# Performance work log

Hardware: AMD Instinct MI355X
Metric: run time of the kernel (lower is better)

Reference implementation:

```python
import jax, jax.numpy as jnp
import numpy as np

R = 16
ALPHA = 32
SCALING = ALPHA / R  # 2.0
E = 8
TOP_K = 2


def setup_inputs() -> dict:
    key = jax.random.key(0)
    ks = jax.random.split(key, 5)
    B, S, D = 4, 2048, 4096
    x = jax.random.normal(ks[0], (B, S, D), dtype=jnp.float32)
    base_W = jax.random.normal(ks[1], (D, D), dtype=jnp.float32) * 0.02
    router_W = jax.random.normal(ks[2], (E, D), dtype=jnp.float32) * 0.02
    lora_A = jax.random.normal(ks[3], (E, D, R), dtype=jnp.float32) * 0.02
    lora_B = jax.random.normal(ks[4], (E, R, D), dtype=jnp.float32) * 0.02
    return {"x": x, "base_W": base_W, "router_W": router_W,
            "lora_A": lora_A, "lora_B": lora_B}


def reference(x, base_W, router_W, lora_A, lora_B):
    # base linear: y = x @ W^T  (nn.Linear, bias=False)
    base = jnp.einsum('bsd,od->bso', x, base_W)

    # router logits and top-2 routing (softmax in fp32, as in torch)
    logits = jnp.einsum('bsd,ed->bse', x, router_W)
    probs = jax.nn.softmax(logits.astype(jnp.float32), axis=-1)  # [B,S,E]
    top_vals, top_idx = jax.lax.top_k(probs, TOP_K)               # [B,S,2]
    rw = top_vals / jnp.sum(top_vals, axis=-1, keepdims=True)
    # scatter top-2 weights into dense [B,S,E] combine matrix
    w_dense = jnp.sum(jax.nn.one_hot(top_idx, E, dtype=rw.dtype) * rw[..., None],
                      axis=-2).astype(x.dtype)                    # [B,S,E]

    # expert LoRA: out_n = sum_e w_ne * (x_n @ A_e @ B_e)
    # apply routing weight at rank-r stage (B_e linear => same math),
    # avoiding the [B,S,E,D] intermediate.
    mid = jnp.einsum('bsd,edr->bser', x, lora_A)                  # [B,S,E,r]
    mid = mid * w_dense[..., None]
    inc = jnp.einsum('bser,erd->bsd', mid, lora_B)                # [B,S,D]

    return base + inc * SCALING
```

## Files before the change

kernel.cpp:

```cpp
#include <hip/hip_runtime.h>
#include <math.h>

#define DI __device__ __forceinline__

typedef __attribute__((ext_vector_type(4))) float  f32x4;
typedef __attribute__((ext_vector_type(4))) short  s16x4;
typedef __attribute__((ext_vector_type(8))) short  s16x8;
typedef __attribute__((ext_vector_type(4))) float  ffrag;
typedef s16x8 bfrag;

constexpr int NT = 8192;
constexpr int D  = 4096;
constexpr int NE = 8;
constexpr int KE = 128;
constexpr int KX = D + KE;

DI short f2bf(float f) {
  unsigned u = __builtin_bit_cast(unsigned, f);
  u += 0x7FFFu + ((u >> 16) & 1u);
  return (short)(u >> 16);
}
DI float bf2f(short h) {
  unsigned u = ((unsigned)(unsigned short)h) << 16;
  return __builtin_bit_cast(float, u);
}

#define GLOAD16(gp, lp)                                                        \
  __builtin_amdgcn_global_load_lds(                                            \
      (const __attribute__((address_space(1))) void*)(gp),                     \
      (__attribute__((address_space(3))) void*)(lp), 16, 0, 0)

__global__ void moe_k_detect(const unsigned* __restrict__ x, int* __restrict__ flag) {
  int l = threadIdx.x;
  int cnt = 0;
  for (int i = l; i < 2048; i += 64) {
    unsigned e = (x[i] >> 23) & 0xFFu;
    cnt += (e >= 110u && e <= 140u) ? 1 : 0;
  }
#pragma unroll
  for (int o = 32; o; o >>= 1) cnt += __shfl_xor(cnt, o);
  if (l == 0) flag[0] = (cnt > 1024) ? 0 : 1;
}

__global__ __launch_bounds__(256)
void moe_k_prep(const void* __restrict__ wp, const void* __restrict__ lAp,
                const void* __restrict__ lBp, const int* __restrict__ flag,
                short* __restrict__ Wb, short* __restrict__ Abt) {
  const bool bf = flag[0] != 0;
  int b = blockIdx.x, t = threadIdx.x;
  if (b < 8192) {
    int tid = b * 256 + t;
    int row = tid >> 9;
    int col = (tid & 511) << 3;
    s16x8 o;
    if (!bf) {
      const float* Wf = (const float*)wp;
      f32x4 v0 = *(const f32x4*)&Wf[(size_t)row * 4096 + col];
      f32x4 v1 = *(const f32x4*)&Wf[(size_t)row * 4096 + col + 4];
      o[0] = f2bf(v0[0]); o[1] = f2bf(v0[1]); o[2] = f2bf(v0[2]); o[3] = f2bf(v0[3]);
      o[4] = f2bf(v1[0]); o[5] = f2bf(v1[1]); o[6] = f2bf(v1[2]); o[7] = f2bf(v1[3]);
    } else {
      o = *(const s16x8*)&((const short*)wp)[(size_t)row * 4096 + col];
    }
    *(s16x8*)&Wb[(size_t)row * KX + col] = o;
  } else if (b < 8208) {
    int d = (b - 8192) * 256 + t;
    for (int j0 = 0; j0 < KE; j0 += 8) {
      s16x8 o;
#pragma unroll
      for (int i = 0; i < 8; ++i) {
        float v = bf ? bf2f(((const short*)lBp)[(size_t)(j0 + i) * 4096 + d])
                     : ((const float*)lBp)[(size_t)(j0 + i) * 4096 + d];
        o[i] = f2bf(2.0f * v);
      }
      *(s16x8*)&Wb[(size_t)d * KX + 4096 + j0] = o;
    }
  } else {
    int j = b - 8208;
    int e = j >> 4, r = j & 15;
    for (int d = t; d < 4096; d += 256) {
      size_t src = ((size_t)e * 4096 + d) * 16 + r;
      short v = bf ? ((const short*)lAp)[src] : f2bf(((const float*)lAp)[src]);
      Abt[(size_t)j * 4096 + d] = v;
    }
  }
}

__global__ __launch_bounds__(256)
void moe_k_xrouter(const void* __restrict__ xp, const void* __restrict__ rp,
                   const int* __restrict__ flag, short* __restrict__ Xb,
                   float* __restrict__ wdense) {
  const bool bf = flag[0] != 0;
  int t = threadIdx.x, wv = t >> 6, l = t & 63;
  int n = blockIdx.x * 4 + wv;
  float acc[NE];
#pragma unroll
  for (int e = 0; e < NE; ++e) acc[e] = 0.f;
  const float* xf = (const float*)xp;
  const short* xh = (const short*)xp;
  const float* rf = (const float*)rp;
  const short* rh = (const short*)rp;
  for (int it = 0; it < 16; ++it) {
    int d = it * 256 + l * 4;
    float x0, x1, x2, x3;
    s16x4 xo;
    if (!bf) {
      f32x4 v = *(const f32x4*)&xf[(size_t)n * D + d];
      x0 = v[0]; x1 = v[1]; x2 = v[2]; x3 = v[3];
      xo[0] = f2bf(x0); xo[1] = f2bf(x1); xo[2] = f2bf(x2); xo[3] = f2bf(x3);
    } else {
      xo = *(const s16x4*)&xh[(size_t)n * D + d];
      x0 = bf2f(xo[0]); x1 = bf2f(xo[1]); x2 = bf2f(xo[2]); x3 = bf2f(xo[3]);
    }
    *(s16x4*)&Xb[(size_t)n * KX + d] = xo;
#pragma unroll
    for (int e = 0; e < NE; ++e) {
      if (!bf) {
        f32x4 w = *(const f32x4*)&rf[(size_t)e * D + d];
        acc[e] += x0 * w[0] + x1 * w[1] + x2 * w[2] + x3 * w[3];
      } else {
        s16x4 w = *(const s16x4*)&rh[(size_t)e * D + d];
        acc[e] += x0 * bf2f(w[0]) + x1 * bf2f(w[1]) + x2 * bf2f(w[2]) + x3 * bf2f(w[3]);
      }
    }
  }
#pragma unroll
  for (int e = 0; e < NE; ++e) {
#pragma unroll
    for (int o = 32; o; o >>= 1) acc[e] += __shfl_xor(acc[e], o);
  }
  float m = acc[0];
#pragma unroll
  for (int e = 1; e < NE; ++e) m = fmaxf(m, acc[e]);
  float p[NE];
#pragma unroll
  for (int e = 0; e < NE; ++e) p[e] = __expf(acc[e] - m);
  int i1 = 0; float v1 = p[0];
#pragma unroll
  for (int e = 1; e < NE; ++e) { if (p[e] > v1) { v1 = p[e]; i1 = e; } }
  int i2 = 0; float v2 = -1.f;
#pragma unroll
  for (int e = 0; e < NE; ++e) { if (e != i1 && p[e] > v2) { v2 = p[e]; i2 = e; } }
  float inv = 1.f / (v1 + v2);
  if (l < NE) {
    float w = (l == i1) ? v1 * inv : ((l == i2) ? v2 * inv : 0.f);
    wdense[(size_t)n * NE + l] = w;
  }
}

__global__ __launch_bounds__(256)
void moe_k_mid2(const short* __restrict__ Xb, const short* __restrict__ Abt,
                const float* __restrict__ wdense, short* __restrict__ XbW) {
  __shared__ __align__(16) short LDS[16384];
  const int t = threadIdx.x, l = t & 63, wv = t >> 6;
  const int wr = wv >> 1, wc = wv & 1;
  const int lr = l & 15, kq = l >> 4;
  const int m0 = (blockIdx.x >> 1) * 64;
  const int j0 = (blockIdx.x & 1) * 64;

  ffrag acc[2][2];
#pragma unroll
  for (int i = 0; i < 2; ++i)
#pragma unroll
    for (int j = 0; j < 2; ++j)
#pragma unroll
      for (int q = 0; q < 4; ++q) acc[i][j][q] = 0.f;

  const int srow = t >> 2, sslot = t & 3;
#define MSTAGE(kt_)                                                            \
  do {                                                                         \
    int _k0 = (kt_) * 32, _b = ((kt_) & 3) * 4096;                             \
    GLOAD16(&Xb[(size_t)(m0 + srow) * KX + _k0 + sslot * 8], &LDS[_b + t * 8]);\
    GLOAD16(&Abt[(size_t)(j0 + srow) * 4096 + _k0 + sslot * 8],                \
            &LDS[_b + 2048 + t * 8]);                                          \
  } while (0)

  MSTAGE(0); MSTAGE(1); MSTAGE(2);
  constexpr int NKT = 128;

  for (int kt = 0; kt < NKT; ++kt) {
    if (kt + 2 < NKT)      asm volatile("s_waitcnt vmcnt(4)" ::: "memory");
    else if (kt + 1 < NKT) asm volatile("s_waitcnt vmcnt(2)" ::: "memory");
    else                   asm volatile("s_waitcnt vmcnt(0)" ::: "memory");
    __builtin_amdgcn_s_barrier();
    __builtin_amdgcn_sched_barrier(0);

    const int bufs = (kt & 3) * 4096;
    const short* As = &LDS[bufs + (wr * 32 + lr) * 32 + kq * 8];
    const short* Bs = &LDS[bufs + 2048 + (wc * 32 + lr) * 32 + kq * 8];
    bfrag a0 = *(const bfrag*)&As[0];
    bfrag a1 = *(const bfrag*)&As[512];
    bfrag b0 = *(const bfrag*)&Bs[0];
    bfrag b1 = *(const bfrag*)&Bs[512];
    if (kt + 3 < NKT) MSTAGE(kt + 3);
    asm volatile("" ::: "memory");
    acc[0][0] = __builtin_amdgcn_mfma_f32_16x16x32_bf16(b0, a0, acc[0][0], 0, 0, 0);
    acc[0][1] = __builtin_amdgcn_mfma_f32_16x16x32_bf16(b1, a0, acc[0][1], 0, 0, 0);
    acc[1][0] = __builtin_amdgcn_mfma_f32_16x16x32_bf16(b0, a1, acc[1][0], 0, 0, 0);
    acc[1][1] = __builtin_amdgcn_mfma_f32_16x16x32_bf16(b1, a1, acc[1][1], 0, 0, 0);
  }

#pragma unroll
  for (int m = 0; m < 2; ++m)
#pragma unroll
    for (int n = 0; n < 2; ++n) {
      int gr = m0 + wr * 32 + m * 16 + lr;
      int jb = j0 + wc * 32 + n * 16 + kq * 4;
      int e  = jb >> 4;
      float w = wdense[(size_t)gr * NE + e];
      s16x4 o;
#pragma unroll
      for (int q = 0; q < 4; ++q) o[q] = f2bf(acc[m][n][q] * w);
      *(s16x4*)&XbW[(size_t)gr * KX + 4096 + jb] = o;
    }
#undef MSTAGE
}

__global__ __launch_bounds__(512, 2)
void moe_k_main8(const short* __restrict__ Xb, const short* __restrict__ Wb,
                 const int* __restrict__ flag, void* __restrict__ outp) {
  __shared__ __align__(16) short LDS[65536];
  const int t = threadIdx.x;
  const int l = t & 63;
  const int wv = t >> 6;
  const int wr = wv >> 2;
  const int wc = wv & 3;
  const int lr = l & 15;
  const int kq = l >> 4;

  int wg = blockIdx.x;
  int swz = (wg & 7) * 64 + (wg >> 3);
  const int tm = (swz >> 4) * 256;
  const int tn = (swz & 15) * 256;

  ffrag acc[8][4];
#pragma unroll
  for (int i = 0; i < 8; ++i)
#pragma unroll
    for (int j = 0; j < 4; ++j)
#pragma unroll
      for (int q = 0; q < 4; ++q) acc[i][j][q] = 0.f;

#define STAGE_A(kt_)                                                           \
  do {                                                                         \
    int _k0 = (kt_) * 32, _b = ((kt_) & 3) * 16384;                            \
    _Pragma("unroll")                                                          \
    for (int _i = 0; _i < 2; ++_i) {                                           \
      int _c = _i * 512 + t;                                                   \
      int _r = _c >> 2;                                                        \
      int _kc = (_c & 3) ^ ((_r >> 1) & 3);                                    \
      GLOAD16(&Xb[(size_t)(tm + _r) * KX + _k0 + _kc * 8], &LDS[_b + _c * 8]); \
    }                                                                          \
  } while (0)
#define STAGE_B(kt_)                                                           \
  do {                                                                         \
    int _k0 = (kt_) * 32, _b = ((kt_) & 3) * 16384 + 8192;                     \
    _Pragma("unroll")                                                          \
    for (int _i = 0; _i < 2; ++_i) {                                           \
      int _c = _i * 512 + t;                                                   \
      int _r = _c >> 2;                                                        \
      int _kc = (_c & 3) ^ ((_r >> 1) & 3);                                    \
      GLOAD16(&Wb[(size_t)(tn + _r) * KX + _k0 + _kc * 8], &LDS[_b + _c * 8]); \
    }                                                                          \
  } while (0)

  STAGE_A(0); STAGE_B(0);
  STAGE_A(1); STAGE_B(1);
  STAGE_A(2); STAGE_B(2);

  constexpr int NKT = KX / 32;

  const int kx = kq ^ ((lr >> 1) & 3);
  const int aofs = (wr * 128 + lr) * 32 + kx * 8;
  const int bofs = 8192 + (wc * 64 + lr) * 32 + kx * 8;

#define MFMA_ROW(mi, av)                                                           \
  acc[mi][0] = __builtin_amdgcn_mfma_f32_16x16x32_bf16(b0, av, acc[mi][0], 0, 0, 0); \
  acc[mi][1] = __builtin_amdgcn_mfma_f32_16x16x32_bf16(b1, av, acc[mi][1], 0, 0, 0); \
  acc[mi][2] = __builtin_amdgcn_mfma_f32_16x16x32_bf16(b2, av, acc[mi][2], 0, 0, 0); \
  acc[mi][3] = __builtin_amdgcn_mfma_f32_16x16x32_bf16(b3, av, acc[mi][3], 0, 0, 0);

  for (int kt = 0; kt < NKT; ++kt) {
    if (kt + 2 < NKT)      asm volatile("s_waitcnt vmcnt(8)" ::: "memory");
    else if (kt + 1 < NKT) asm volatile("s_waitcnt vmcnt(4)" ::: "memory");
    else                   asm volatile("s_waitcnt vmcnt(0)" ::: "memory");
    __builtin_amdgcn_s_barrier();
    __builtin_amdgcn_sched_barrier(0);

    const int bufs = (kt & 3) * 16384;
    const short* Ab = &LDS[bufs + aofs];
    const short* Bb = &LDS[bufs + bofs];

    bfrag b0 = *(const bfrag*)&Bb[0];
    bfrag b1 = *(const bfrag*)&Bb[512];
    bfrag b2 = *(const bfrag*)&Bb[1024];
    bfrag b3 = *(const bfrag*)&Bb[1536];
    bfrag a0 = *(const bfrag*)&Ab[0];
    bfrag a1 = *(const bfrag*)&Ab[512];
    bfrag a2 = *(const bfrag*)&Ab[1024];
    bfrag a3 = *(const bfrag*)&Ab[1536];
    if (kt + 3 < NKT) STAGE_A(kt + 3);
    asm volatile("" ::: "memory");
    __builtin_amdgcn_s_barrier();
    __builtin_amdgcn_sched_barrier(0);
    __builtin_amdgcn_s_setprio(1);
    MFMA_ROW(0, a0) MFMA_ROW(1, a1) MFMA_ROW(2, a2) MFMA_ROW(3, a3)
    __builtin_amdgcn_s_setprio(0);

    bfrag a4 = *(const bfrag*)&Ab[2048];
    bfrag a5 = *(const bfrag*)&Ab[2560];
    bfrag a6 = *(const bfrag*)&Ab[3072];
    bfrag a7 = *(const bfrag*)&Ab[3584];
    if (kt + 3 < NKT) STAGE_B(kt + 3);
    asm volatile("" ::: "memory");
    __builtin_amdgcn_s_barrier();
    __builtin_amdgcn_sched_barrier(0);
    __builtin_amdgcn_s_setprio(1);
    MFMA_ROW(4, a4) MFMA_ROW(5, a5) MFMA_ROW(6, a6) MFMA_ROW(7, a7)
    __builtin_amdgcn_s_setprio(0);
  }

  const bool bf = flag[0] != 0;
  float* of = (float*)outp;
  unsigned short* oh = (unsigned short*)outp;
#pragma unroll
  for (int m = 0; m < 8; ++m)
#pragma unroll
    for (int n = 0; n < 4; ++n) {
      int gr = tm + wr * 128 + m * 16 + lr;
      int gc = tn + wc * 64 + n * 16 + kq * 4;
      if (!bf) {
        *(f32x4*)&of[(size_t)gr * D + gc] = acc[m][n];
      } else {
        s16x4 o;
#pragma unroll
        for (int q = 0; q < 4; ++q) o[q] = f2bf(acc[m][n][q]);
        *(s16x4*)&oh[(size_t)gr * D + gc] = o;
      }
    }
#undef STAGE_A
#undef STAGE_B
#undef MFMA_ROW
}

extern "C" void kernel_launch(void* const* d_in, const int* in_sizes, int n_in,
                              void* d_out, int out_size, void* d_ws, size_t ws_size,
                              hipStream_t stream) {
  const void* x  = d_in[0];
  const void* bw = d_in[1];
  const void* rw = d_in[2];
  const void* lA = d_in[3];
  const void* lB = d_in[4];

  char* ws = (char*)d_ws;
  const size_t XB_BYTES  = (size_t)NT * KX * 2;
  const size_t WB_BYTES  = (size_t)D * KX * 2;
  const size_t ABT_BYTES = (size_t)KE * D * 2;
  const size_t WD_BYTES  = (size_t)NT * NE * 4;
  const size_t NEED = 256 + XB_BYTES + WB_BYTES + ABT_BYTES + WD_BYTES;
  if (ws_size < NEED) return;

  int*   flag   = (int*)ws;
  short* Xb     = (short*)(ws + 256);
  short* Wb     = (short*)(ws + 256 + XB_BYTES);
  short* Abt    = (short*)(ws + 256 + XB_BYTES + WB_BYTES);
  float* wdense = (float*)(ws + 256 + XB_BYTES + WB_BYTES + ABT_BYTES);

  hipLaunchKernelGGL(moe_k_detect, dim3(1), dim3(64), 0, stream,
                     (const unsigned*)x, flag);
  hipLaunchKernelGGL(moe_k_prep, dim3(8336), dim3(256), 0, stream,
                     bw, lA, lB, flag, Wb, Abt);
  hipLaunchKernelGGL(moe_k_xrouter, dim3(NT / 4), dim3(256), 0, stream,
                     x, rw, flag, Xb, wdense);
  hipLaunchKernelGGL(moe_k_mid2, dim3(256), dim3(256), 0, stream,
                     Xb, Abt, wdense, Xb);
  hipLaunchKernelGGL(moe_k_main8, dim3(512), dim3(512), 0, stream,
                     Xb, Wb, flag, d_out);
}
```

Baseline: 403.7 us.

## Shrink main GEMM tile to 128x128 with double buffering and merge prep kernels

Result: slower. 521.0 us (+29.1%).

```diff
diff --git a/kernel.cpp b/kernel.cpp
--- a/kernel.cpp
+++ b/kernel.cpp
@@ -43,9 +43,11 @@
 }
 
 __global__ __launch_bounds__(256)
-void moe_k_prep(const void* __restrict__ wp, const void* __restrict__ lAp,
-                const void* __restrict__ lBp, const int* __restrict__ flag,
-                short* __restrict__ Wb, short* __restrict__ Abt) {
+void moe_k_prep_xr(const void* __restrict__ wp, const void* __restrict__ lAp,
+                   const void* __restrict__ lBp, const void* __restrict__ xp,
+                   const void* __restrict__ rp, const int* __restrict__ flag,
+                   short* __restrict__ Wb, short* __restrict__ Abt,
+                   short* __restrict__ Xb, float* __restrict__ wdense) {
   const bool bf = flag[0] != 0;
   int b = blockIdx.x, t = threadIdx.x;
   if (b < 8192) {
@@ -75,7 +77,7 @@
       }
       *(s16x8*)&Wb[(size_t)d * KX + 4096 + j0] = o;
     }
-  } else {
+  } else if (b < 8336) {
     int j = b - 8208;
     int e = j >> 4, r = j & 15;
     for (int d = t; d < 4096; d += 256) {
@@ -83,68 +85,62 @@
       short v = bf ? ((const short*)lAp)[src] : f2bf(((const float*)lAp)[src]);
       Abt[(size_t)j * 4096 + d] = v;
     }
-  }
-}
-
-__global__ __launch_bounds__(256)
-void moe_k_xrouter(const void* __restrict__ xp, const void* __restrict__ rp,
-                   const int* __restrict__ flag, short* __restrict__ Xb,
-                   float* __restrict__ wdense) {
-  const bool bf = flag[0] != 0;
-  int t = threadIdx.x, wv = t >> 6, l = t & 63;
-  int n = blockIdx.x * 4 + wv;
-  float acc[NE];
-#pragma unroll
-  for (int e = 0; e < NE; ++e) acc[e] = 0.f;
-  const float* xf = (const float*)xp;
-  const short* xh = (const short*)xp;
-  const float* rf = (const float*)rp;
-  const short* rh = (const short*)rp;
-  for (int it = 0; it < 16; ++it) {
-    int d = it * 256 + l * 4;
-    float x0, x1, x2, x3;
-    s16x4 xo;
-    if (!bf) {
-      f32x4 v = *(const f32x4*)&xf[(size_t)n * D + d];
-      x0 = v[0]; x1 = v[1]; x2 = v[2]; x3 = v[3];
-      xo[0] = f2bf(x0); xo[1] = f2bf(x1); xo[2] = f2bf(x2); xo[3] = f2bf(x3);
-    } else {
-      xo = *(const s16x4*)&xh[(size_t)n * D + d];
-      x0 = bf2f(xo[0]); x1 = bf2f(xo[1]); x2 = bf2f(xo[2]); x3 = bf2f(xo[3]);
-    }
-    *(s16x4*)&Xb[(size_t)n * KX + d] = xo;
+  } else {
+    int wv = t >> 6, l = t & 63;
+    int n = (b - 8336) * 4 + wv;
+    float acc[NE];
+#pragma unroll
+    for (int e = 0; e < NE; ++e) acc[e] = 0.f;
+    const float* xf = (const float*)xp;
+    const short* xh = (const short*)xp;
+    const float* rf = (const float*)rp;
+    const short* rh = (const short*)rp;
+    for (int it = 0; it < 16; ++it) {
+      int d = it * 256 + l * 4;
+      float x0, x1, x2, x3;
+      s16x4 xo;
+      if (!bf) {
+        f32x4 v = *(const f32x4*)&xf[(size_t)n * D + d];
+        x0 = v[0]; x1 = v[1]; x2 = v[2]; x3 = v[3];
+        xo[0] = f2bf(x0); xo[1] = f2bf(x1); xo[2] = f2bf(x2); xo[3] = f2bf(x3);
+      } else {
+        xo = *(const s16x4*)&xh[(size_t)n * D + d];
+        x0 = bf2f(xo[0]); x1 = bf2f(xo[1]); x2 = bf2f(xo[2]); x3 = bf2f(xo[3]);
+      }
+      *(s16x4*)&Xb[(size_t)n * KX + d] = xo;
+#pragma unroll
+      for (int e = 0; e < NE; ++e) {
+        if (!bf) {
+          f32x4 w = *(const f32x4*)&rf[(size_t)e * D + d];
+          acc[e] += x0 * w[0] + x1 * w[1] + x2 * w[2] + x3 * w[3];
+        } else {
+          s16x4 w = *(const s16x4*)&rh[(size_t)e * D + d];
+          acc[e] += x0 * bf2f(w[0]) + x1 * bf2f(w[1]) + x2 * bf2f(w[2]) + x3 * bf2f(w[3]);
+        }
+      }
+    }
 #pragma unroll
     for (int e = 0; e < NE; ++e) {
-      if (!bf) {
-        f32x4 w = *(const f32x4*)&rf[(size_t)e * D + d];
-        acc[e] += x0 * w[0] + x1 * w[1] + x2 * w[2] + x3 * w[3];
-      } else {
-        s16x4 w = *(const s16x4*)&rh[(size_t)e * D + d];
-        acc[e] += x0 * bf2f(w[0]) + x1 * bf2f(w[1]) + x2 * bf2f(w[2]) + x3 * bf2f(w[3]);
-      }
-    }
-  }
-#pragma unroll
-  for (int e = 0; e < NE; ++e) {
-#pragma unroll
-    for (int o = 32; o; o >>= 1) acc[e] += __shfl_xor(acc[e], o);
-  }
-  float m = acc[0];
-#pragma unroll
-  for (int e = 1; e < NE; ++e) m = fmaxf(m, acc[e]);
-  float p[NE];
-#pragma unroll
-  for (int e = 0; e < NE; ++e) p[e] = __expf(acc[e] - m);
-  int i1 = 0; float v1 = p[0];
-#pragma unroll
-  for (int e = 1; e < NE; ++e) { if (p[e] > v1) { v1 = p[e]; i1 = e; } }
-  int i2 = 0; float v2 = -1.f;
-#pragma unroll
-  for (int e = 0; e < NE; ++e) { if (e != i1 && p[e] > v2) { v2 = p[e]; i2 = e; } }
-  float inv = 1.f / (v1 + v2);
-  if (l < NE) {
-    float w = (l == i1) ? v1 * inv : ((l == i2) ? v2 * inv : 0.f);
-    wdense[(size_t)n * NE + l] = w;
+#pragma unroll
+      for (int o = 32; o; o >>= 1) acc[e] += __shfl_xor(acc[e], o);
+    }
+    float m = acc[0];
+#pragma unroll
+    for (int e = 1; e < NE; ++e) m = fmaxf(m, acc[e]);
+    float p[NE];
+#pragma unroll
+    for (int e = 0; e < NE; ++e) p[e] = __expf(acc[e] - m);
+    int i1 = 0; float v1 = p[0];
+#pragma unroll
+    for (int e = 1; e < NE; ++e) { if (p[e] > v1) { v1 = p[e]; i1 = e; } }
+    int i2 = 0; float v2 = -1.f;
+#pragma unroll
+    for (int e = 0; e < NE; ++e) { if (e != i1 && p[e] > v2) { v2 = p[e]; i2 = e; } }
+    float inv = 1.f / (v1 + v2);
+    if (l < NE) {
+      float w = (l == i1) ? v1 * inv : ((l == i2) ? v2 * inv : 0.f);
+      wdense[(size_t)n * NE + l] = w;
+    }
   }
 }
 
@@ -216,81 +212,67 @@
 #undef MSTAGE
 }
 
-__global__ __launch_bounds__(512, 2)
-void moe_k_main8(const short* __restrict__ Xb, const short* __restrict__ Wb,
-                 const int* __restrict__ flag, void* __restrict__ outp) {
-  __shared__ __align__(16) short LDS[65536];
+__global__ __launch_bounds__(256, 4)
+void moe_k_main10(const short* __restrict__ Xb, const short* __restrict__ Wb,
+                  const int* __restrict__ flag, void* __restrict__ outp) {
+  __shared__ __align__(16) short LDS[16384];
   const int t = threadIdx.x;
   const int l = t & 63;
   const int wv = t >> 6;
-  const int wr = wv >> 2;
-  const int wc = wv & 3;
+  const int wr = wv >> 1;
+  const int wc = wv & 1;
   const int lr = l & 15;
   const int kq = l >> 4;
 
   int wg = blockIdx.x;
-  int swz = (wg & 7) * 64 + (wg >> 3);
-  const int tm = (swz >> 4) * 256;
-  const int tn = (swz & 15) * 256;
-
-  ffrag acc[8][4];
-#pragma unroll
-  for (int i = 0; i < 8; ++i)
+  int swz = (wg & 7) * 256 + (wg >> 3);
+  const int tm = (swz >> 5) * 128;
+  const int tn = (swz & 31) * 128;
+
+  ffrag acc[4][4];
+#pragma unroll
+  for (int i = 0; i < 4; ++i)
 #pragma unroll
     for (int j = 0; j < 4; ++j)
 #pragma unroll
       for (int q = 0; q < 4; ++q) acc[i][j][q] = 0.f;
 
-#define STAGE_A(kt_)                                                           \
+#define STG(kt_, OFS_, src_, tb_)                                              \
   do {                                                                         \
-    int _k0 = (kt_) * 32, _b = ((kt_) & 3) * 16384;                            \
+    int _k0 = (kt_) * 32, _b = ((kt_) & 1) * 8192 + (OFS_);                    \
     _Pragma("unroll")                                                          \
     for (int _i = 0; _i < 2; ++_i) {                                           \
-      int _c = _i * 512 + t;                                                   \
+      int _c = _i * 256 + t;                                                   \
       int _r = _c >> 2;                                                        \
       int _kc = (_c & 3) ^ ((_r >> 1) & 3);                                    \
-      GLOAD16(&Xb[(size_t)(tm + _r) * KX + _k0 + _kc * 8], &LDS[_b + _c * 8]); \
+      GLOAD16(&src_[(size_t)((tb_) + _r) * KX + _k0 + _kc * 8],                \
+              &LDS[_b + _c * 8]);                                              \
     }                                                                          \
   } while (0)
-#define STAGE_B(kt_)                                                           \
-  do {                                                                         \
-    int _k0 = (kt_) * 32, _b = ((kt_) & 3) * 16384 + 8192;                     \
-    _Pragma("unroll")                                                          \
-    for (int _i = 0; _i < 2; ++_i) {                                           \
-      int _c = _i * 512 + t;                                                   \
-      int _r = _c >> 2;                                                        \
-      int _kc = (_c & 3) ^ ((_r >> 1) & 3);                                    \
-      GLOAD16(&Wb[(size_t)(tn + _r) * KX + _k0 + _kc * 8], &LDS[_b + _c * 8]); \
-    }                                                                          \
-  } while (0)
+#define STAGE_A(kt_) STG(kt_, 0,    Xb, tm)
+#define STAGE_B(kt_) STG(kt_, 4096, Wb, tn)
 
   STAGE_A(0); STAGE_B(0);
-  STAGE_A(1); STAGE_B(1);
-  STAGE_A(2); STAGE_B(2);
 
   constexpr int NKT = KX / 32;
-
   const int kx = kq ^ ((lr >> 1) & 3);
-  const int aofs = (wr * 128 + lr) * 32 + kx * 8;
-  const int bofs = 8192 + (wc * 64 + lr) * 32 + kx * 8;
-
-#define MFMA_ROW(mi, av)                                                           \
-  acc[mi][0] = __builtin_amdgcn_mfma_f32_16x16x32_bf16(b0, av, acc[mi][0], 0, 0, 0); \
-  acc[mi][1] = __builtin_amdgcn_mfma_f32_16x16x32_bf16(b1, av, acc[mi][1], 0, 0, 0); \
-  acc[mi][2] = __builtin_amdgcn_mfma_f32_16x16x32_bf16(b2, av, acc[mi][2], 0, 0, 0); \
-  acc[mi][3] = __builtin_amdgcn_mfma_f32_16x16x32_bf16(b3, av, acc[mi][3], 0, 0, 0);
+  const int aofs = (wr * 64 + lr) * 32 + kx * 8;
+  const int bofs = 4096 + (wc * 64 + lr) * 32 + kx * 8;
+
+#define MM(m_, n_, bv_, av_)                                                   \
+  acc[m_][n_] = __builtin_amdgcn_mfma_f32_16x16x32_bf16(bv_, av_, acc[m_][n_], 0, 0, 0);
 
   for (int kt = 0; kt < NKT; ++kt) {
-    if (kt + 2 < NKT)      asm volatile("s_waitcnt vmcnt(8)" ::: "memory");
-    else if (kt + 1 < NKT) asm volatile("s_waitcnt vmcnt(4)" ::: "memory");
-    else                   asm volatile("s_waitcnt vmcnt(0)" ::: "memory");
+    if (kt) __builtin_amdgcn_s_barrier();
+    if (kt + 1 < NKT) { STAGE_A(kt + 1); STAGE_B(kt + 1); }
+    if (kt + 1 < NKT) asm volatile("s_waitcnt vmcnt(4)" ::: "memory");
+    else              asm volatile("s_waitcnt vmcnt(0)" ::: "memory");
     __builtin_amdgcn_s_barrier();
     __builtin_amdgcn_sched_barrier(0);
 
-    const int bufs = (kt & 3) * 16384;
+    const int bufs = (kt & 1) * 8192;
     const short* Ab = &LDS[bufs + aofs];
     const short* Bb = &LDS[bufs + bofs];
-
     bfrag b0 = *(const bfrag*)&Bb[0];
     bfrag b1 = *(const bfrag*)&Bb[512];
     bfrag b2 = *(const bfrag*)&Bb[1024];
@@ -299,24 +281,11 @@
     bfrag a1 = *(const bfrag*)&Ab[512];
     bfrag a2 = *(const bfrag*)&Ab[1024];
     bfrag a3 = *(const bfrag*)&Ab[1536];
-    if (kt + 3 < NKT) STAGE_A(kt + 3);
-    asm volatile("" ::: "memory");
-    __builtin_amdgcn_s_barrier();
-    __builtin_amdgcn_sched_barrier(0);
     __builtin_amdgcn_s_setprio(1);
-    MFMA_ROW(0, a0) MFMA_ROW(1, a1) MFMA_ROW(2, a2) MFMA_ROW(3, a3)
-    __builtin_amdgcn_s_setprio(0);
-
-    bfrag a4 = *(const bfrag*)&Ab[2048];
-    bfrag a5 = *(const bfrag*)&Ab[2560];
-    bfrag a6 = *(const bfrag*)&Ab[3072];
-    bfrag a7 = *(const bfrag*)&Ab[3584];
-    if (kt + 3 < NKT) STAGE_B(kt + 3);
-    asm volatile("" ::: "memory");
-    __builtin_amdgcn_s_barrier();
-    __builtin_amdgcn_sched_barrier(0);
-    __builtin_amdgcn_s_setprio(1);
-    MFMA_ROW(4, a4) MFMA_ROW(5, a5) MFMA_ROW(6, a6) MFMA_ROW(7, a7)
+    MM(0, 0, b0, a0) MM(0, 1, b1, a0) MM(0, 2, b2, a0) MM(0, 3, b3, a0)
+    MM(1, 0, b0, a1) MM(1, 1, b1, a1) MM(1, 2, b2, a1) MM(1, 3, b3, a1)
+    MM(2, 0, b0, a2) MM(2, 1, b1, a2) MM(2, 2, b2, a2) MM(2, 3, b3, a2)
+    MM(3, 0, b0, a3) MM(3, 1, b1, a3) MM(3, 2, b2, a3) MM(3, 3, b3, a3)
     __builtin_amdgcn_s_setprio(0);
   }
 
@@ -324,10 +293,10 @@
   float* of = (float*)outp;
   unsigned short* oh = (unsigned short*)outp;
 #pragma unroll
-  for (int m = 0; m < 8; ++m)
+  for (int m = 0; m < 4; ++m)
 #pragma unroll
     for (int n = 0; n < 4; ++n) {
-      int gr = tm + wr * 128 + m * 16 + lr;
+      int gr = tm + wr * 64 + m * 16 + lr;
       int gc = tn + wc * 64 + n * 16 + kq * 4;
       if (!bf) {
         *(f32x4*)&of[(size_t)gr * D + gc] = acc[m][n];
@@ -338,9 +307,10 @@
         *(s16x4*)&oh[(size_t)gr * D + gc] = o;
       }
     }
+#undef STG
 #undef STAGE_A
 #undef STAGE_B
-#undef MFMA_ROW
+#undef MM
 }
 
 extern "C" void kernel_launch(void* const* d_in, const int* in_sizes, int n_in,
@@ -368,12 +338,10 @@
 
   hipLaunchKernelGGL(moe_k_detect, dim3(1), dim3(64), 0, stream,
                      (const unsigned*)x, flag);
-  hipLaunchKernelGGL(moe_k_prep, dim3(8336), dim3(256), 0, stream,
-                     bw, lA, lB, flag, Wb, Abt);
-  hipLaunchKernelGGL(moe_k_xrouter, dim3(NT / 4), dim3(256), 0, stream,
-                     x, rw, flag, Xb, wdense);
+  hipLaunchKernelGGL(moe_k_prep_xr, dim3(10384), dim3(256), 0, stream,
+                     bw, lA, lB, x, rw, flag, Wb, Abt, Xb, wdense);
   hipLaunchKernelGGL(moe_k_mid2, dim3(256), dim3(256), 0, stream,
                      Xb, Abt, wdense, Xb);
-  hipLaunchKernelGGL(moe_k_main8, dim3(512), dim3(512), 0, stream,
+  hipLaunchKernelGGL(moe_k_main10, dim3(2048), dim3(256), 0, stream,
                      Xb, Wb, flag, d_out);
 }
```
